# Optimization experiments

Measured on AMD Instinct MI355X. Metric: run time of the kernel, lower is better.

## Reference

```python
import jax, jax.numpy as jnp
import numpy as np

SIGMA = 1.0
MU = 1.0
STRIKE = 3.0
N_STEPS = 256
BATCH = 131072


def setup_inputs() -> dict:
    key = jax.random.key(0)
    ks = jax.random.split(key, 4)

    def lin(k, o, i):
        # equinox Linear-style uniform init in [-1/sqrt(i), 1/sqrt(i)]
        lim = 1.0 / np.sqrt(i)
        return jax.random.uniform(k, (o, i), jnp.float32, -lim, lim)

    return {
        "noise": jax.random.normal(ks[0], (N_STEPS, BATCH), jnp.float32),
        "ts": jnp.linspace(0.0, 1.0, N_STEPS + 1, dtype=jnp.float32),
        "w": jnp.float32(0.9),  # E[max(S1 - K, 0)] Monte-Carlo constant
        "W1": lin(ks[1], 32, 2), "b1": jnp.zeros((32,), jnp.float32),
        "W2": lin(ks[2], 32, 32), "b2": jnp.zeros((32,), jnp.float32),
        "W3": lin(ks[3], 1, 32), "b3": jnp.zeros((1,), jnp.float32),
    }


def reference(noise, ts, w, W1, b1, W2, b2, W3, b3):
    # Holding strategy MLP: in=[t, s] (2) -> 32 -> 32 -> 1, silu/silu/sigmoid
    def holding(t, s):  # s: [B] -> h: [B]
        x = jnp.stack([jnp.broadcast_to(t, s.shape), s], axis=-1)  # [B,2]
        a = jax.nn.silu(x @ W1.T + b1)
        a = jax.nn.silu(a @ W2.T + b2)
        return jax.nn.sigmoid(a @ W3.T + b3)[:, 0]

    def drift(t, y):  # y: [B,2] -> [B,2]
        s = y[:, 0]
        h = holding(t, s)
        return jnp.stack([MU * s, MU * s * h], axis=-1)

    def diffusion(t, y):  # scalar Brownian noise: diffusion vector [B,2]
        s = y[:, 0]
        h = holding(t, s)
        return jnp.stack([SIGMA * s, SIGMA * s * h], axis=-1)

    dts = jnp.diff(ts)                      # [N]
    dWs = noise * jnp.sqrt(dts)[:, None]    # [N,B] Brownian increments

    def step(y, xs):
        t, dt, dW = xs                      # dW: [B]
        f = drift(t, y)
        g = diffusion(t, y)
        # Milstein correction: directional derivative (Dg . g) via jvp
        _, dg = jax.jvp(lambda yy: diffusion(t, yy), (y,), (g,))
        y1 = (y + f * dt + g * dW[:, None]
              + 0.5 * dg * (dW * dW - dt)[:, None])  # Ito Milstein
        return y1, None

    B = noise.shape[1]
    y0 = jnp.broadcast_to(jnp.array([1.0, 0.0], jnp.float32), (B, 2))
    yT, _ = jax.lax.scan(step, y0, (ts[:-1], dts, dWs))

    s1 = yT[:, 0]
    hedging_pnl = yT[:, 1]
    z = jnp.maximum(0.0, s1 - STRIKE)
    return (z - hedging_pnl - w) ** 2  # [B] per-path loss
```

## Files before the change

### kernel.cpp

```cpp
#include <hip/hip_runtime.h>
#include <hip/hip_fp16.h>
#include <math.h>

#define BATCH 131072
#define NSTEPS 256
#define LGN 7
#define NPTS 128
#define ZSPAN 12.0f
#define ZLO 6.0f
#define ZSCALE (NPTS / ZSPAN)
#define DZ (ZSPAN / NPTS)
#define MU_C 0.72134752044448170367f
#define SD_C 1.4426950408889634f

using f32x2 = __attribute__((ext_vector_type(2))) float;

__device__ __forceinline__ float fast_exp(float x) {
    return __builtin_amdgcn_exp2f(x * 1.44269504088896340736f);
}
__device__ __forceinline__ float fast_rcp(float x) {
    return __builtin_amdgcn_rcpf(x);
}
__device__ __forceinline__ float sigmoidf_fast(float x) {
    return fast_rcp(1.0f + fast_exp(-x));
}

#define REP32(M) M(0) M(1) M(2) M(3) M(4) M(5) M(6) M(7) \
                 M(8) M(9) M(10) M(11) M(12) M(13) M(14) M(15) \
                 M(16) M(17) M(18) M(19) M(20) M(21) M(22) M(23) \
                 M(24) M(25) M(26) M(27) M(28) M(29) M(30) M(31)

#define REP16(M) M(0) M(1) M(2) M(3) M(4) M(5) M(6) M(7) \
                 M(8) M(9) M(10) M(11) M(12) M(13) M(14) M(15)

#define REP16P(M, P) M(0,P) M(1,P) M(2,P) M(3,P) M(4,P) M(5,P) M(6,P) M(7,P) \
                     M(8,P) M(9,P) M(10,P) M(11,P) M(12,P) M(13,P) M(14,P) M(15,P)

#define MLP_BODY(W1r, B1, W2r, B2, W3r, b3v, t, s, sd, H, HACC) \
    { \
        const float __t = (t), __s = (s), __sd = (sd); \
        f32x2 acc2 = {(b3v), 0.0f}; \
        REP32(MLP_L1) \
        REP32(MLP_ROW) \
        H = sigmoidf_fast(acc2.x); \
        HACC = acc2.y; \
    }

#define MLP_L1(j) f32x2 at##j; { \
    const float2 wv = W1r[j]; \
    const float z  = fmaf(wv.x, __t, fmaf(wv.y, __s, B1[j])); \
    const float zd = wv.y * __sd; \
    const float sg = sigmoidf_fast(z); \
    const float da = sg * (1.0f + z * (1.0f - sg)); \
    at##j = (f32x2){z * sg, da * zd}; }

#define MLP_ROW(j) { \
    const float4 q0 = W2r[(j) * 8 + 0]; \
    const float4 q1 = W2r[(j) * 8 + 1]; \
    const float4 q2 = W2r[(j) * 8 + 2]; \
    const float4 q3 = W2r[(j) * 8 + 3]; \
    const float4 q4 = W2r[(j) * 8 + 4]; \
    const float4 q5 = W2r[(j) * 8 + 5]; \
    const float4 q6 = W2r[(j) * 8 + 6]; \
    const float4 q7 = W2r[(j) * 8 + 7]; \
    f32x2 zza = {B2[j], 0.0f}; \
    f32x2 zzb = {0.0f, 0.0f}; \
    zza += (f32x2){q0.x, q0.x} * at0;  zzb += (f32x2){q0.y, q0.y} * at1; \
    zza += (f32x2){q0.z, q0.z} * at2;  zzb += (f32x2){q0.w, q0.w} * at3; \
    zza += (f32x2){q1.x, q1.x} * at4;  zzb += (f32x2){q1.y, q1.y} * at5; \
    zza += (f32x2){q1.z, q1.z} * at6;  zzb += (f32x2){q1.w, q1.w} * at7; \
    zza += (f32x2){q2.x, q2.x} * at8;  zzb += (f32x2){q2.y, q2.y} * at9; \
    zza += (f32x2){q2.z, q2.z} * at10; zzb += (f32x2){q2.w, q2.w} * at11; \
    zza += (f32x2){q3.x, q3.x} * at12; zzb += (f32x2){q3.y, q3.y} * at13; \
    zza += (f32x2){q3.z, q3.z} * at14; zzb += (f32x2){q3.w, q3.w} * at15; \
    zza += (f32x2){q4.x, q4.x} * at16; zzb += (f32x2){q4.y, q4.y} * at17; \
    zza += (f32x2){q4.z, q4.z} * at18; zzb += (f32x2){q4.w, q4.w} * at19; \
    zza += (f32x2){q5.x, q5.x} * at20; zzb += (f32x2){q5.y, q5.y} * at21; \
    zza += (f32x2){q5.z, q5.z} * at22; zzb += (f32x2){q5.w, q5.w} * at23; \
    zza += (f32x2){q6.x, q6.x} * at24; zzb += (f32x2){q6.y, q6.y} * at25; \
    zza += (f32x2){q6.z, q6.z} * at26; zzb += (f32x2){q6.w, q6.w} * at27; \
    zza += (f32x2){q7.x, q7.x} * at28; zzb += (f32x2){q7.y, q7.y} * at29; \
    zza += (f32x2){q7.z, q7.z} * at30; zzb += (f32x2){q7.w, q7.w} * at31; \
    const f32x2 zzt = zza + zzb; \
    const float zv  = zzt.x; \
    const float sg  = sigmoidf_fast(zv); \
    const float da  = sg * (1.0f + zv * (1.0f - sg)); \
    const float w3  = W3r[j]; \
    acc2 += (f32x2){w3, w3} * (f32x2){zv * sg, da * zzt.y}; \
}

__global__ __launch_bounds__(256) void table_eval_kernel(
    const float* __restrict__ ts,
    const float* __restrict__ W1, const float* __restrict__ b1,
    const float* __restrict__ W2, const float* __restrict__ b2,
    const float* __restrict__ W3, const float* __restrict__ b3,
    unsigned int* __restrict__ A)
{
    __shared__ __align__(16) float sW1[64];
    __shared__ float sb1[32];
    __shared__ __align__(16) float sW2[1024];
    __shared__ float sb2[32];
    __shared__ float sW3[32];
    __shared__ float sb3[1];

    const int tid = threadIdx.x;
    for (int i = tid; i < 1024; i += 256) sW2[i] = W2[i];
    if (tid < 64) sW1[tid] = W1[tid];
    if (tid < 32) { sb1[tid] = b1[tid]; sb2[tid] = b2[tid]; sW3[tid] = W3[tid]; }
    if (tid == 0) sb3[0] = b3[0];
    __syncthreads();

    const float2* W1r = (const float2*)sW1;
    const float*  B1  = sb1;
    const float4* W2r = (const float4*)sW2;
    const float*  B2  = sb2;
    const float*  W3r = sW3;
    const float   b3v = sb3[0];

    const int gid = blockIdx.x * 256 + tid;
    const int st = gid >> LGN;
    const int k  = gid & (NPTS - 1);

    const float t  = ts[st];
    const float mu = MU_C * t;
    const float sd = SD_C * __builtin_sqrtf(t) + 1e-4f;
    const float zz = fmaf((float)k, DZ, -ZLO);
    const float s  = __builtin_amdgcn_exp2f(fmaf(zz, sd, mu));

    float h, hacc;
    MLP_BODY(W1r, B1, W2r, B2, W3r, b3v, t, s, 1.0f, h, hacc)

    const float q = h * (1.0f - h) * hacc * s;
    __half2 p = __floats2half2_rn(h, q);
    A[gid] = *(unsigned int*)&p;
}

__global__ __launch_bounds__(256) void pack_kernel(
    const unsigned int* __restrict__ A, uint2* __restrict__ T2)
{
    const int gid = blockIdx.x * 256 + threadIdx.x;
    const int k = gid & (NPTS - 1);
    const unsigned int a = A[gid];
    const unsigned int b = A[gid + (k < NPTS - 1 ? 1 : 0)];
    T2[gid] = make_uint2(a, b);
}

__global__ __launch_bounds__(256, 1) void path_kernel(
    const float* __restrict__ noise,
    const float* __restrict__ ts,
    const float* __restrict__ wq,
    const uint2* __restrict__ T2,
    float* __restrict__ out)
{
    __shared__ float4 sdt4[NSTEPS];
    __shared__ float  scr[NSTEPS];
    const int tid = threadIdx.x;
    if (tid < NSTEPS) {
        const float t0  = ts[tid];
        const float dtv = ts[tid + 1] - t0;
        const float sdv = SD_C * __builtin_sqrtf(t0) + 1e-4f;
        const float wp  = fast_rcp(sdv) * ZSCALE;
        const float cp  = ZLO * ZSCALE - MU_C * t0 * wp;
        sdt4[tid] = make_float4(dtv, __builtin_sqrtf(dtv), cp, wp);
        scr[tid]  = 0.69314718056f * fast_rcp(wp);
    }
    __syncthreads();

    const int gid = blockIdx.x * 256 + tid;
    const float* np_ = noise + gid;
    const float umax = (float)NPTS - 1.001f;

    float s   = 1.0f;
    float pnl = 0.0f;

    #define NLA(k) float nA##k = np_[(size_t)(k) * BATCH];
    #define NLB(k) float nB##k = np_[(size_t)(16 + k) * BATCH];
    REP16(NLA)
    REP16(NLB)
    #undef NLA
    #undef NLB

    #define CHK(k, NP) \
        const float4 dq##k = sdt4[base + k]; \
        const float  cr##k = scr[base + k]; \
        const float dW##k  = NP##k * dq##k.y; \
        const float mil##k = 0.5f * fmaf(dW##k, dW##k, -dq##k.x); \
        const float Af##k  = dq##k.x + dW##k + mil##k; \
        const float sv##k  = s; \
        s = fmaf(s, Af##k, s); \
        const float x##k = __builtin_amdgcn_logf(sv##k); \
        const float u##k = fminf(fmaxf(fmaf(x##k, dq##k.w, dq##k.z), 0.0f), umax); \
        const int   i0##k = (int)u##k; \
        const float f##k  = u##k - (float)i0##k; \
        unsigned long long E##k = \
            ((const unsigned long long*)(T2 + ((size_t)(base + k) << LGN)))[i0##k];

    #define NPF(k, NP) NP##k = np_[(size_t)(pfb + k) * BATCH];

    #define PNK(k) { \
        const uint2 eu = __builtin_bit_cast(uint2, E##k); \
        const float2 a0 = __half22float2(*(const __half2*)&eu.x); \
        const float2 a1 = __half22float2(*(const __half2*)&eu.y); \
        const float uu = f##k; \
        const float m  = uu * uu; \
        const float n  = m * uu; \
        const float dh = a1.x - a0.x; \
        const float ba = fmaf(-2.0f, n, 3.0f * m);             \
        const float bb = fmaf(-2.0f, m, uu) + n;               \
        const float bc = n - m;                                \
        const float hh = fmaf(dh, ba, a0.x) \
                       + cr##k * fmaf(a0.y, bb, a1.y * bc); \
        const float qq = fmaf(uu, a1.y - a0.y, a0.y); \
        const float v  = fmaf(qq, mil##k, hh * Af##k); \
        pnl = fmaf(sv##k, v, pnl); }

    #define BODY(cexpr, NP) { \
        const int base = (cexpr) * 16; \
        const int pfb  = min(base + 32, NSTEPS - 16); \
        REP16P(CHK, NP) \
        __builtin_amdgcn_sched_barrier(0); \
        REP16P(NPF, NP) \
        asm volatile("" : "+v"(E0), "+v"(E1), "+v"(E2), "+v"(E3), \
                          "+v"(E4), "+v"(E5), "+v"(E6), "+v"(E7)); \
        asm volatile("" : "+v"(E8),  "+v"(E9),  "+v"(E10), "+v"(E11), \
                          "+v"(E12), "+v"(E13), "+v"(E14), "+v"(E15)); \
        __builtin_amdgcn_sched_barrier(0); \
        REP16(PNK) \
    }

    #pragma unroll 1
    for (int cc = 0; cc < NSTEPS / 32; ++cc) {
        BODY(cc * 2,     nA)
        BODY(cc * 2 + 1, nB)
    }

    #undef BODY
    #undef PNK
    #undef NPF
    #undef CHK

    const float z = fmaxf(0.0f, s - 3.0f);
    const float d = z - pnl - wq[0];
    out[gid] = d * d;
}

__global__ __launch_bounds__(256, 3) void deep_hedging_direct(
    const float* __restrict__ noise, const float* __restrict__ ts,
    const float* __restrict__ w,
    const float* __restrict__ W1, const float* __restrict__ b1,
    const float* __restrict__ W2, const float* __restrict__ b2,
    const float* __restrict__ W3, const float* __restrict__ b3,
    float* __restrict__ out)
{
    __shared__ __align__(16) float sW1[64];
    __shared__ float sb1[32];
    __shared__ __align__(16) float sW2[1024];
    __shared__ float sb2[32];
    __shared__ float sW3[32];
    __shared__ float sb3w[2];
    __shared__ float sts[NSTEPS + 1];

    const int tid = threadIdx.x;
    for (int i = tid; i < 1024; i += 256) sW2[i] = W2[i];
    if (tid < 64) sW1[tid] = W1[tid];
    if (tid < 32) { sb1[tid] = b1[tid]; sb2[tid] = b2[tid]; sW3[tid] = W3[tid]; }
    if (tid == 0) { sb3w[0] = b3[0]; sb3w[1] = w[0]; }
    for (int i = tid; i < NSTEPS + 1; i += 256) sts[i] = ts[i];
    __syncthreads();

    const int gid = blockIdx.x * 256 + tid;
    const float* np_ = noise + gid;

    float s   = 1.0f;
    float pnl = 0.0f;
    const float b3v = sb3w[0];
    const float wv_ = sb3w[1];

    #pragma unroll 1
    for (int st = 0; st < NSTEPS; ++st) {
        int zr = 0;
        asm volatile("" : "+v"(zr));
        const float2* W1r = (const float2*)sW1 + zr;
        const float*  B1  = sb1 + zr;
        const float4* W2r = (const float4*)sW2 + zr;
        const float*  B2  = sb2 + zr;
        const float*  W3r = sW3 + zr;

        const float t  = sts[st];
        const float dt = sts[st + 1] - t;
        const float dW = np_[(size_t)st * BATCH] * __builtin_sqrtf(dt);
        const float sd = s;

        float h, hacc;
        MLP_BODY(W1r, B1, W2r, B2, W3r, b3v, t, s, sd, h, hacc)
        const float hd = h * (1.0f - h) * hacc;

        const float mil = 0.5f * (dW * dW - dt);
        const float g1  = s * h;
        const float dg1 = fmaf(sd, h, s * hd);
        const float snew = s + s * dt + s * dW + sd * mil;
        pnl = pnl + g1 * dt + g1 * dW + dg1 * mil;
        s = snew;
    }

    const float z = fmaxf(0.0f, s - 3.0f);
    const float d = z - pnl - wv_;
    out[gid] = d * d;
}

extern "C" void kernel_launch(void* const* d_in, const int* in_sizes, int n_in,
                              void* d_out, int out_size, void* d_ws, size_t ws_size,
                              hipStream_t stream) {
    const float* noise = (const float*)d_in[0];
    const float* ts    = (const float*)d_in[1];
    const float* w     = (const float*)d_in[2];
    const float* W1    = (const float*)d_in[3];
    const float* b1    = (const float*)d_in[4];
    const float* W2    = (const float*)d_in[5];
    const float* b2    = (const float*)d_in[6];
    const float* W3    = (const float*)d_in[7];
    const float* b3    = (const float*)d_in[8];
    float* out = (float*)d_out;

    const size_t nA   = (size_t)NSTEPS * NPTS;
    const size_t need = nA * (sizeof(unsigned int) + sizeof(uint2));

    if (ws_size >= need) {
        unsigned int* A = (unsigned int*)d_ws;
        uint2* T2 = (uint2*)((char*)d_ws + nA * sizeof(unsigned int));

        dim3 tb(256), tg(nA / 256);
        table_eval_kernel<<<tg, tb, 0, stream>>>(ts, W1, b1, W2, b2, W3, b3, A);
        pack_kernel<<<tg, tb, 0, stream>>>(A, T2);
        dim3 pb(256), pg(BATCH / 256);
        path_kernel<<<pg, pb, 0, stream>>>(noise, ts, w, T2, out);
    } else {
        dim3 grid(BATCH / 256), block(256);
        deep_hedging_direct<<<grid, block, 0, stream>>>(noise, ts, w, W1, b1,
                                                        W2, b2, W3, b3, out);
    }
}
```

Before: 61.93 us.

## Fuse table packing into eval kernel and batch two 16-step chunks per phase

The table evaluation kernel now writes each half2 entry straight into the paired (a, b) layout, duplicating it into the neighbour slot, so the separate pack kernel launch and its intermediate buffer go away. The path kernel now issues all 32 table gathers for a 32-step chunk before any interpolation, instead of two 16-step phases, giving more loads in flight. It also precomputes s*Af and s*mil per step to shorten the pnl update and moves the scr load into the consume phase. The cost is higher register pressure from holding 32 gathered entries at once.

```diff
diff --git a/kernel.cpp b/kernel.cpp
--- a/kernel.cpp
+++ b/kernel.cpp
@@ -32,9 +32,6 @@
 
 #define REP16(M) M(0) M(1) M(2) M(3) M(4) M(5) M(6) M(7) \
                  M(8) M(9) M(10) M(11) M(12) M(13) M(14) M(15)
-
-#define REP16P(M, P) M(0,P) M(1,P) M(2,P) M(3,P) M(4,P) M(5,P) M(6,P) M(7,P) \
-                     M(8,P) M(9,P) M(10,P) M(11,P) M(12,P) M(13,P) M(14,P) M(15,P)
 
 #define MLP_BODY(W1r, B1, W2r, B2, W3r, b3v, t, s, sd, H, HACC) \
     { \
@@ -94,7 +91,7 @@
     const float* __restrict__ W1, const float* __restrict__ b1,
     const float* __restrict__ W2, const float* __restrict__ b2,
     const float* __restrict__ W3, const float* __restrict__ b3,
-    unsigned int* __restrict__ A)
+    unsigned int* __restrict__ W)
 {
     __shared__ __align__(16) float sW1[64];
     __shared__ float sb1[32];
@@ -132,17 +129,11 @@
 
     const float q = h * (1.0f - h) * hacc * s;
     __half2 p = __floats2half2_rn(h, q);
-    A[gid] = *(unsigned int*)&p;
-}
-
-__global__ __launch_bounds__(256) void pack_kernel(
-    const unsigned int* __restrict__ A, uint2* __restrict__ T2)
-{
-    const int gid = blockIdx.x * 256 + threadIdx.x;
-    const int k = gid & (NPTS - 1);
-    const unsigned int a = A[gid];
-    const unsigned int b = A[gid + (k < NPTS - 1 ? 1 : 0)];
-    T2[gid] = make_uint2(a, b);
+    const unsigned int pv = *(unsigned int*)&p;
+
+    W[2 * gid] = pv;
+    if (k > 0)         W[2 * gid - 1] = pv;
+    if (k == NPTS - 1) W[2 * gid + 1] = pv;
 }
 
 __global__ __launch_bounds__(256, 1) void path_kernel(
@@ -173,68 +164,84 @@
     float s   = 1.0f;
     float pnl = 0.0f;
 
-    #define NLA(k) float nA##k = np_[(size_t)(k) * BATCH];
-    #define NLB(k) float nB##k = np_[(size_t)(16 + k) * BATCH];
-    REP16(NLA)
-    REP16(NLB)
-    #undef NLA
-    #undef NLB
-
-    #define CHK(k, NP) \
-        const float4 dq##k = sdt4[base + k]; \
-        const float  cr##k = scr[base + k]; \
-        const float dW##k  = NP##k * dq##k.y; \
-        const float mil##k = 0.5f * fmaf(dW##k, dW##k, -dq##k.x); \
-        const float Af##k  = dq##k.x + dW##k + mil##k; \
-        const float sv##k  = s; \
-        s = fmaf(s, Af##k, s); \
-        const float x##k = __builtin_amdgcn_logf(sv##k); \
-        const float u##k = fminf(fmaxf(fmaf(x##k, dq##k.w, dq##k.z), 0.0f), umax); \
-        const int   i0##k = (int)u##k; \
-        const float f##k  = u##k - (float)i0##k; \
-        unsigned long long E##k = \
-            ((const unsigned long long*)(T2 + ((size_t)(base + k) << LGN)))[i0##k];
-
-    #define NPF(k, NP) NP##k = np_[(size_t)(pfb + k) * BATCH];
-
-    #define PNK(k) { \
-        const uint2 eu = __builtin_bit_cast(uint2, E##k); \
+    #define NL0(k) float nA##k = np_[(size_t)(k) * BATCH]; \
+                   float nB##k = np_[(size_t)(16 + k) * BATCH];
+    REP16(NL0)
+    #undef NL0
+
+    #define CHK(k, G, NPv, BASE) \
+        const float4 dq##G##k = sdt4[(BASE) + k]; \
+        const float dW##G##k  = NPv##k * dq##G##k.y; \
+        const float mil##G##k = 0.5f * fmaf(dW##G##k, dW##G##k, -dq##G##k.x); \
+        const float Af##G##k  = dq##G##k.x + dW##G##k + mil##G##k; \
+        const float sv##G##k  = s; \
+        s = fmaf(s, Af##G##k, s); \
+        const float P##G##k = sv##G##k * Af##G##k; \
+        const float Q##G##k = sv##G##k * mil##G##k; \
+        const float x##G##k = __builtin_amdgcn_logf(sv##G##k); \
+        const float u##G##k = \
+            fminf(fmaxf(fmaf(x##G##k, dq##G##k.w, dq##G##k.z), 0.0f), umax); \
+        const int   i0##G##k = (int)u##G##k; \
+        const float f##G##k  = u##G##k - (float)i0##G##k; \
+        unsigned long long E##G##k = \
+            ((const unsigned long long*)(T2 + ((size_t)((BASE) + k) << LGN)))[i0##G##k];
+
+    #define NPF(k, NPv, PFB) NPv##k = np_[(size_t)((PFB) + k) * BATCH];
+
+    #define PNK(k, G, BASE) { \
+        const uint2 eu = __builtin_bit_cast(uint2, E##G##k); \
         const float2 a0 = __half22float2(*(const __half2*)&eu.x); \
         const float2 a1 = __half22float2(*(const __half2*)&eu.y); \
-        const float uu = f##k; \
+        const float cr = scr[(BASE) + k]; \
+        const float uu = f##G##k; \
         const float m  = uu * uu; \
         const float n  = m * uu; \
         const float dh = a1.x - a0.x; \
         const float ba = fmaf(-2.0f, n, 3.0f * m);             \
         const float bb = fmaf(-2.0f, m, uu) + n;               \
         const float bc = n - m;                                \
-        const float hh = fmaf(dh, ba, a0.x) \
-                       + cr##k * fmaf(a0.y, bb, a1.y * bc); \
+        const float hh = fmaf(dh, ba, a0.x) + cr * fmaf(a0.y, bb, a1.y * bc); \
         const float qq = fmaf(uu, a1.y - a0.y, a0.y); \
-        const float v  = fmaf(qq, mil##k, hh * Af##k); \
-        pnl = fmaf(sv##k, v, pnl); }
-
-    #define BODY(cexpr, NP) { \
-        const int base = (cexpr) * 16; \
-        const int pfb  = min(base + 32, NSTEPS - 16); \
-        REP16P(CHK, NP) \
-        __builtin_amdgcn_sched_barrier(0); \
-        REP16P(NPF, NP) \
-        asm volatile("" : "+v"(E0), "+v"(E1), "+v"(E2), "+v"(E3), \
-                          "+v"(E4), "+v"(E5), "+v"(E6), "+v"(E7)); \
-        asm volatile("" : "+v"(E8),  "+v"(E9),  "+v"(E10), "+v"(E11), \
-                          "+v"(E12), "+v"(E13), "+v"(E14), "+v"(E15)); \
-        __builtin_amdgcn_sched_barrier(0); \
-        REP16(PNK) \
-    }
+        pnl = fmaf(hh, P##G##k, fmaf(qq, Q##G##k, pnl)); }
+
+    #define CHA(k) CHK(k, A, nA, baseA)
+    #define CHB(k) CHK(k, B, nB, baseB)
+    #define NPA(k) NPF(k, nA, pfA)
+    #define NPB(k) NPF(k, nB, pfB)
+    #define PNA(k) PNK(k, A, baseA)
+    #define PNB(k) PNK(k, B, baseB)
 
     #pragma unroll 1
     for (int cc = 0; cc < NSTEPS / 32; ++cc) {
-        BODY(cc * 2,     nA)
-        BODY(cc * 2 + 1, nB)
-    }
-
-    #undef BODY
+        const int baseA = cc * 32;
+        const int baseB = cc * 32 + 16;
+        const int pfA = min(baseA + 32, NSTEPS - 16);
+        const int pfB = min(baseB + 32, NSTEPS - 16);
+
+        REP16(CHA)
+        REP16(CHB)
+        __builtin_amdgcn_sched_barrier(0);
+        REP16(NPA)
+        REP16(NPB)
+        asm volatile("" : "+v"(EA0), "+v"(EA1), "+v"(EA2),  "+v"(EA3),
+                          "+v"(EA4), "+v"(EA5), "+v"(EA6),  "+v"(EA7));
+        asm volatile("" : "+v"(EA8), "+v"(EA9), "+v"(EA10), "+v"(EA11),
+                          "+v"(EA12),"+v"(EA13),"+v"(EA14), "+v"(EA15));
+        asm volatile("" : "+v"(EB0), "+v"(EB1), "+v"(EB2),  "+v"(EB3),
+                          "+v"(EB4), "+v"(EB5), "+v"(EB6),  "+v"(EB7));
+        asm volatile("" : "+v"(EB8), "+v"(EB9), "+v"(EB10), "+v"(EB11),
+                          "+v"(EB12),"+v"(EB13),"+v"(EB14), "+v"(EB15));
+        __builtin_amdgcn_sched_barrier(0);
+        REP16(PNA)
+        REP16(PNB)
+    }
+
+    #undef CHA
+    #undef CHB
+    #undef NPA
+    #undef NPB
+    #undef PNA
+    #undef PNB
     #undef PNK
     #undef NPF
     #undef CHK
@@ -323,15 +330,14 @@
     float* out = (float*)d_out;
 
     const size_t nA   = (size_t)NSTEPS * NPTS;
-    const size_t need = nA * (sizeof(unsigned int) + sizeof(uint2));
+    const size_t need = nA * sizeof(uint2);
 
     if (ws_size >= need) {
-        unsigned int* A = (unsigned int*)d_ws;
-        uint2* T2 = (uint2*)((char*)d_ws + nA * sizeof(unsigned int));
+        uint2* T2 = (uint2*)d_ws;
 
         dim3 tb(256), tg(nA / 256);
-        table_eval_kernel<<<tg, tb, 0, stream>>>(ts, W1, b1, W2, b2, W3, b3, A);
-        pack_kernel<<<tg, tb, 0, stream>>>(A, T2);
+        table_eval_kernel<<<tg, tb, 0, stream>>>(ts, W1, b1, W2, b2, W3, b3,
+                                                 (unsigned int*)T2);
         dim3 pb(256), pg(BATCH / 256);
         path_kernel<<<pg, pb, 0, stream>>>(noise, ts, w, T2, out);
     } else {
```

After: 61.77 us. No clear change (-0.3%).

## Split time scan into four segments via precomputed multiplicative prefix products

Applied to the files above, without the earlier changes.

The path recurrence s_{k+1}=s_k(1+A_k) is linear, so a new prod_kernel computes the per-segment products of (1+A_k) for the first three 64-step segments. That lets seg_kernel launch four times as many blocks, each scanning only 64 steps, instead of one thread walking all 256 steps. Partial PnL sums go to a workspace buffer and fin_kernel reduces them. The pack kernel is dropped because table_eval now writes the paired interpolation entries directly. In exchange the first three quarters of the noise array are read twice, and there are extra kernel launches and workspace traffic.

```diff
diff --git a/kernel.cpp b/kernel.cpp
--- a/kernel.cpp
+++ b/kernel.cpp
@@ -4,6 +4,8 @@
 
 #define BATCH 131072
 #define NSTEPS 256
+#define SEGLEN 64
+#define NSEG 4
 #define LGN 7
 #define NPTS 128
 #define ZSPAN 12.0f
@@ -30,11 +32,7 @@
                  M(16) M(17) M(18) M(19) M(20) M(21) M(22) M(23) \
                  M(24) M(25) M(26) M(27) M(28) M(29) M(30) M(31)
 
-#define REP16(M) M(0) M(1) M(2) M(3) M(4) M(5) M(6) M(7) \
-                 M(8) M(9) M(10) M(11) M(12) M(13) M(14) M(15)
-
-#define REP16P(M, P) M(0,P) M(1,P) M(2,P) M(3,P) M(4,P) M(5,P) M(6,P) M(7,P) \
-                     M(8,P) M(9,P) M(10,P) M(11,P) M(12,P) M(13,P) M(14,P) M(15,P)
+#define REP8(M) M(0) M(1) M(2) M(3) M(4) M(5) M(6) M(7)
 
 #define MLP_BODY(W1r, B1, W2r, B2, W3r, b3v, t, s, sd, H, HACC) \
     { \
@@ -94,7 +92,7 @@
     const float* __restrict__ W1, const float* __restrict__ b1,
     const float* __restrict__ W2, const float* __restrict__ b2,
     const float* __restrict__ W3, const float* __restrict__ b3,
-    unsigned int* __restrict__ A)
+    unsigned int* __restrict__ W)
 {
     __shared__ __align__(16) float sW1[64];
     __shared__ float sb1[32];
@@ -132,32 +130,65 @@
 
     const float q = h * (1.0f - h) * hacc * s;
     __half2 p = __floats2half2_rn(h, q);
-    A[gid] = *(unsigned int*)&p;
-}
-
-__global__ __launch_bounds__(256) void pack_kernel(
-    const unsigned int* __restrict__ A, uint2* __restrict__ T2)
-{
-    const int gid = blockIdx.x * 256 + threadIdx.x;
-    const int k = gid & (NPTS - 1);
-    const unsigned int a = A[gid];
-    const unsigned int b = A[gid + (k < NPTS - 1 ? 1 : 0)];
-    T2[gid] = make_uint2(a, b);
-}
-
-__global__ __launch_bounds__(256, 1) void path_kernel(
+    const unsigned int pv = *(unsigned int*)&p;
+
+    W[2 * gid] = pv;
+    if (k > 0)         W[2 * gid - 1] = pv;
+    if (k == NPTS - 1) W[2 * gid + 1] = pv;
+}
+
+__global__ __launch_bounds__(256) void prod_kernel(
     const float* __restrict__ noise,
     const float* __restrict__ ts,
-    const float* __restrict__ wq,
+    float* __restrict__ P)
+{
+    __shared__ float2 sdt[SEGLEN];
+    const int g    = blockIdx.x >> 9;
+    const int pblk = blockIdx.x & 511;
+    const int tid  = threadIdx.x;
+    const int sbase = g * SEGLEN;
+
+    if (tid < SEGLEN) {
+        const float t0 = ts[sbase + tid];
+        const float dtv = ts[sbase + tid + 1] - t0;
+        sdt[tid] = make_float2(dtv, __builtin_sqrtf(dtv));
+    }
+    __syncthreads();
+
+    const int path = pblk * 256 + tid;
+    const float* np_ = noise + (size_t)sbase * BATCH + path;
+
+    float prod = 1.0f;
+    #pragma unroll 8
+    for (int k = 0; k < SEGLEN; ++k) {
+        const float2 d = sdt[k];
+        const float dW  = np_[(size_t)k * BATCH] * d.y;
+        const float mil = 0.5f * fmaf(dW, dW, -d.x);
+        const float A   = d.x + dW + mil;
+        prod = fmaf(prod, A, prod);
+    }
+    P[(size_t)g * BATCH + path] = prod;
+}
+
+__global__ __launch_bounds__(256, 4) void seg_kernel(
+    const float* __restrict__ noise,
+    const float* __restrict__ ts,
     const uint2* __restrict__ T2,
+    const float* __restrict__ P,
+    float* __restrict__ pnlb,
+    float* __restrict__ sT,
     float* __restrict__ out)
 {
-    __shared__ float4 sdt4[NSTEPS];
-    __shared__ float  scr[NSTEPS];
-    const int tid = threadIdx.x;
-    if (tid < NSTEPS) {
-        const float t0  = ts[tid];
-        const float dtv = ts[tid + 1] - t0;
+    __shared__ float4 sdt4[SEGLEN];
+    __shared__ float  scr[SEGLEN];
+    const int g    = blockIdx.x >> 9;
+    const int pblk = blockIdx.x & 511;
+    const int tid  = threadIdx.x;
+    const int sbase = g * SEGLEN;
+
+    if (tid < SEGLEN) {
+        const float t0  = ts[sbase + tid];
+        const float dtv = ts[sbase + tid + 1] - t0;
         const float sdv = SD_C * __builtin_sqrtf(t0) + 1e-4f;
         const float wp  = fast_rcp(sdv) * ZSCALE;
         const float cp  = ZLO * ZSCALE - MU_C * t0 * wp;
@@ -166,82 +197,88 @@
     }
     __syncthreads();
 
-    const int gid = blockIdx.x * 256 + tid;
-    const float* np_ = noise + gid;
+    const int path = pblk * 256 + tid;
+    const float* np_ = noise + (size_t)sbase * BATCH + path;
     const float umax = (float)NPTS - 1.001f;
 
-    float s   = 1.0f;
+    float s = 1.0f;
+    if (g > 0) s = P[path];
+    if (g > 1) s *= P[BATCH + path];
+    if (g > 2) s *= P[2 * BATCH + path];
     float pnl = 0.0f;
 
-    #define NLA(k) float nA##k = np_[(size_t)(k) * BATCH];
-    #define NLB(k) float nB##k = np_[(size_t)(16 + k) * BATCH];
-    REP16(NLA)
-    REP16(NLB)
-    #undef NLA
-    #undef NLB
-
-    #define CHK(k, NP) \
-        const float4 dq##k = sdt4[base + k]; \
-        const float  cr##k = scr[base + k]; \
-        const float dW##k  = NP##k * dq##k.y; \
-        const float mil##k = 0.5f * fmaf(dW##k, dW##k, -dq##k.x); \
-        const float Af##k  = dq##k.x + dW##k + mil##k; \
-        const float sv##k  = s; \
-        s = fmaf(s, Af##k, s); \
-        const float x##k = __builtin_amdgcn_logf(sv##k); \
-        const float u##k = fminf(fmaxf(fmaf(x##k, dq##k.w, dq##k.z), 0.0f), umax); \
-        const int   i0##k = (int)u##k; \
-        const float f##k  = u##k - (float)i0##k; \
-        unsigned long long E##k = \
-            ((const unsigned long long*)(T2 + ((size_t)(base + k) << LGN)))[i0##k];
-
-    #define NPF(k, NP) NP##k = np_[(size_t)(pfb + k) * BATCH];
-
-    #define PNK(k) { \
-        const uint2 eu = __builtin_bit_cast(uint2, E##k); \
-        const float2 a0 = __half22float2(*(const __half2*)&eu.x); \
-        const float2 a1 = __half22float2(*(const __half2*)&eu.y); \
-        const float uu = f##k; \
-        const float m  = uu * uu; \
-        const float n  = m * uu; \
-        const float dh = a1.x - a0.x; \
-        const float ba = fmaf(-2.0f, n, 3.0f * m);             \
-        const float bb = fmaf(-2.0f, m, uu) + n;               \
-        const float bc = n - m;                                \
-        const float hh = fmaf(dh, ba, a0.x) \
-                       + cr##k * fmaf(a0.y, bb, a1.y * bc); \
-        const float qq = fmaf(uu, a1.y - a0.y, a0.y); \
-        const float v  = fmaf(qq, mil##k, hh * Af##k); \
-        pnl = fmaf(sv##k, v, pnl); }
-
-    #define BODY(cexpr, NP) { \
-        const int base = (cexpr) * 16; \
-        const int pfb  = min(base + 32, NSTEPS - 16); \
-        REP16P(CHK, NP) \
-        __builtin_amdgcn_sched_barrier(0); \
-        REP16P(NPF, NP) \
-        asm volatile("" : "+v"(E0), "+v"(E1), "+v"(E2), "+v"(E3), \
-                          "+v"(E4), "+v"(E5), "+v"(E6), "+v"(E7)); \
-        asm volatile("" : "+v"(E8),  "+v"(E9),  "+v"(E10), "+v"(E11), \
-                          "+v"(E12), "+v"(E13), "+v"(E14), "+v"(E15)); \
-        __builtin_amdgcn_sched_barrier(0); \
-        REP16(PNK) \
-    }
+    #define NLD0(k) float n##k = np_[(size_t)(k) * BATCH];
+    REP8(NLD0)
+    #undef NLD0
 
     #pragma unroll 1
-    for (int cc = 0; cc < NSTEPS / 32; ++cc) {
-        BODY(cc * 2,     nA)
-        BODY(cc * 2 + 1, nB)
-    }
-
-    #undef BODY
-    #undef PNK
-    #undef NPF
-    #undef CHK
-
-    const float z = fmaxf(0.0f, s - 3.0f);
+    for (int cc = 0; cc < SEGLEN / 8; ++cc) {
+        const int coff = cc * 8;
+        const int pfo  = min(coff + 8, SEGLEN - 8);
+        const float* nb = np_ + (size_t)pfo * BATCH;
+
+        #define NPF(k) const float m##k = nb[(size_t)(k) * BATCH];
+        REP8(NPF)
+        #undef NPF
+
+        #define CHK(k) \
+            const float4 dq##k = sdt4[coff + k]; \
+            const float dW##k  = n##k * dq##k.y; \
+            const float mil##k = 0.5f * fmaf(dW##k, dW##k, -dq##k.x); \
+            const float Af##k  = dq##k.x + dW##k + mil##k; \
+            const float sv##k  = s; \
+            s = fmaf(s, Af##k, s); \
+            const float Pv##k = sv##k * Af##k; \
+            const float Qv##k = sv##k * mil##k; \
+            const float x##k = __builtin_amdgcn_logf(sv##k); \
+            const float u##k = \
+                fminf(fmaxf(fmaf(x##k, dq##k.w, dq##k.z), 0.0f), umax); \
+            const int   i0##k = (int)u##k; \
+            const float f##k  = u##k - (float)i0##k; \
+            const uint2 E##k = \
+                T2[((size_t)(sbase + coff + k) << LGN) + i0##k];
+        REP8(CHK)
+        #undef CHK
+
+        #define PNK(k) { \
+            const float2 a0 = __half22float2(*(const __half2*)&E##k.x); \
+            const float2 a1 = __half22float2(*(const __half2*)&E##k.y); \
+            const float cr = scr[coff + k]; \
+            const float uu = f##k; \
+            const float m  = uu * uu; \
+            const float n  = m * uu; \
+            const float dh = a1.x - a0.x; \
+            const float ba = fmaf(-2.0f, n, 3.0f * m); \
+            const float bb = fmaf(-2.0f, m, uu) + n; \
+            const float bc = n - m; \
+            const float hh = fmaf(dh, ba, a0.x) + cr * fmaf(a0.y, bb, a1.y * bc); \
+            const float qq = fmaf(uu, a1.y - a0.y, a0.y); \
+            pnl = fmaf(hh, Pv##k, fmaf(qq, Qv##k, pnl)); }
+        REP8(PNK)
+        #undef PNK
+
+        #define NRT(k) n##k = m##k;
+        REP8(NRT)
+        #undef NRT
+    }
+
+    if (g == 0) {
+        out[path] = pnl;
+    } else {
+        pnlb[(size_t)(g - 1) * BATCH + path] = pnl;
+    }
+    if (g == 3) sT[path] = s;
+}
+
+__global__ __launch_bounds__(256) void fin_kernel(
+    const float* __restrict__ pnlb, const float* __restrict__ sT,
+    const float* __restrict__ wq, float* __restrict__ out)
+{
+    const int p = blockIdx.x * 256 + threadIdx.x;
+    const float pnl = out[p] + pnlb[p] + pnlb[BATCH + p] + pnlb[2 * BATCH + p];
+    const float z = fmaxf(0.0f, sT[p] - 3.0f);
     const float d = z - pnl - wq[0];
-    out[gid] = d * d;
+    out[p] = d * d;
 }
 
 __global__ __launch_bounds__(256, 3) void deep_hedging_direct(
@@ -322,18 +359,23 @@
     const float* b3    = (const float*)d_in[8];
     float* out = (float*)d_out;
 
-    const size_t nA   = (size_t)NSTEPS * NPTS;
-    const size_t need = nA * (sizeof(unsigned int) + sizeof(uint2));
+    const size_t tblB = (size_t)NSTEPS * NPTS * sizeof(uint2);
+    const size_t pB   = (size_t)3 * BATCH * sizeof(float);
+    const size_t need = tblB + 2 * pB + (size_t)BATCH * sizeof(float);
 
     if (ws_size >= need) {
-        unsigned int* A = (unsigned int*)d_ws;
-        uint2* T2 = (uint2*)((char*)d_ws + nA * sizeof(unsigned int));
-
-        dim3 tb(256), tg(nA / 256);
-        table_eval_kernel<<<tg, tb, 0, stream>>>(ts, W1, b1, W2, b2, W3, b3, A);
-        pack_kernel<<<tg, tb, 0, stream>>>(A, T2);
-        dim3 pb(256), pg(BATCH / 256);
-        path_kernel<<<pg, pb, 0, stream>>>(noise, ts, w, T2, out);
+        uint2* T2   = (uint2*)d_ws;
+        float* P    = (float*)((char*)d_ws + tblB);
+        float* pnlb = (float*)((char*)d_ws + tblB + pB);
+        float* sT   = (float*)((char*)d_ws + tblB + 2 * pB);
+
+        dim3 b(256);
+        table_eval_kernel<<<dim3(NSTEPS * NPTS / 256), b, 0, stream>>>(
+            ts, W1, b1, W2, b2, W3, b3, (unsigned int*)T2);
+        prod_kernel<<<dim3(3 * BATCH / 256), b, 0, stream>>>(noise, ts, P);
+        seg_kernel<<<dim3(4 * BATCH / 256), b, 0, stream>>>(
+            noise, ts, T2, P, pnlb, sT, out);
+        fin_kernel<<<dim3(BATCH / 256), b, 0, stream>>>(pnlb, sT, w, out);
     } else {
         dim3 grid(BATCH / 256), block(256);
         deep_hedging_direct<<<grid, block, 0, stream>>>(noise, ts, w, W1, b1,
```

Measured after the change: 72.64 us. 17.3% more time.
